# Performance work log

Hardware: AMD Instinct MI355X
Metric: run time of the kernel (lower is better)

Reference implementation:

```python
import jax, jax.numpy as jnp
import numpy as np
import math

NUM_HEADS = 8
SR_RATIO = 2
LN_EPS = 1e-5


def setup_inputs() -> dict:
    key = jax.random.key(0)
    ks = jax.random.split(key, 8)
    B, H, W, C = 2, 64, 64, 512
    N = H * W
    M = (H // SR_RATIO) * (W // SR_RATIO)  # 1024, K/V feature dim after SR reshape
    units = C  # num_heads * head_dim
    s = 0.02
    return {
        "x": jax.random.normal(ks[0], (B, N, C), jnp.float32),
        "Wq": jax.random.normal(ks[1], (C, units), jnp.float32) * s,
        "bq": jnp.zeros((units,), jnp.float32),
        "Wconv": jax.random.normal(ks[2], (C, C, SR_RATIO, SR_RATIO), jnp.float32) * s,  # OIHW
        "bconv": jnp.zeros((C,), jnp.float32),
        "gamma": jnp.ones((M,), jnp.float32),
        "beta": jnp.zeros((M,), jnp.float32),
        "Wkv": jax.random.normal(ks[3], (M, 2 * units), jnp.float32) * s,
        "bkv": jnp.zeros((2 * units,), jnp.float32),
        "Wproj": jax.random.normal(ks[4], (units, C), jnp.float32) * s,
        "bproj": jnp.zeros((C,), jnp.float32),
        "H": H,
        "W": W,
    }


def reference(x, Wq, bq, Wconv, bconv, gamma, beta, Wkv, bkv, Wproj, bproj, H, W):
    B, N, C = x.shape
    nh = NUM_HEADS
    hd = C // nh
    units = nh * hd
    sr = SR_RATIO

    # Q: [B, nh, N, hd]
    q = (x @ Wq + bq).reshape(B, N, nh, hd).transpose(0, 2, 1, 3)

    # Spatial reduction on K/V: x -> [B, C, H, W] -> conv(stride=sr) -> [B, C, H/sr, W/sr]
    xi = x.transpose(0, 2, 1).reshape(B, C, H, W)
    xc = jax.lax.conv_general_dilated(
        xi, Wconv, window_strides=(sr, sr), padding="VALID",
        dimension_numbers=("NCHW", "OIHW", "NCHW"))
    xc = xc + bconv[None, :, None, None]
    x_ = xc.reshape(B, C, -1)  # [B, C, M]; K/V seq len = C, feature dim = M
    mu = jnp.mean(x_, axis=-1, keepdims=True)
    var = jnp.mean(jnp.square(x_ - mu), axis=-1, keepdims=True)
    x_ = (x_ - mu) * jax.lax.rsqrt(var + LN_EPS) * gamma + beta

    # KV: [B, C, 2*units] -> [2, B, nh, C, hd]
    kv = (x_ @ Wkv + bkv).reshape(B, C, 2, nh, hd).transpose(2, 0, 3, 1, 4)
    k, v = kv[0], kv[1]  # each [B, nh, C, hd]

    attn = jnp.einsum("bhnd,bhmd->bhnm", q, k) / jnp.asarray(math.sqrt(hd), x.dtype)
    attn = jax.nn.softmax(attn, axis=-1)  # [B, nh, N, C]

    out = jnp.einsum("bhnm,bhmd->bhnd", attn, v)  # [B, nh, N, hd]
    # Faithful to original: transpose to [B, nh, hd, N] then row-major reshape to [B, N, units]
    out = out.transpose(0, 1, 3, 2).reshape(B, -1, units)
    out = out @ Wproj + bproj  # [B, N, C]
    return out
```

## Files before the change

### kernel.cpp

```cpp
#include <hip/hip_runtime.h>


#define B_    2
#define NTOK  4096
#define C_    512
#define MSP   1024
#define NH    8
#define HD    64

typedef __attribute__((ext_vector_type(8))) short short8;
typedef __attribute__((ext_vector_type(4))) short short4v;
typedef __attribute__((ext_vector_type(4))) float f32x4;

__device__ __forceinline__ unsigned short f2bf(float f) {
    unsigned u = __builtin_bit_cast(unsigned, f);
    u += 0x7FFFu + ((u >> 16) & 1u);
    return (unsigned short)(u >> 16);
}

__global__ __launch_bounds__(256) void convert_bf16(
    const float* __restrict__ in, unsigned short* __restrict__ out, int n8)
{
    int i = blockIdx.x * 256 + threadIdx.x;
    if (i >= n8) return;
    float4 a = ((const float4*)in)[2 * i];
    float4 b = ((const float4*)in)[2 * i + 1];
    short8 o;
    o[0] = (short)f2bf(a.x); o[1] = (short)f2bf(a.y);
    o[2] = (short)f2bf(a.z); o[3] = (short)f2bf(a.w);
    o[4] = (short)f2bf(b.x); o[5] = (short)f2bf(b.y);
    o[6] = (short)f2bf(b.z); o[7] = (short)f2bf(b.w);
    ((short8*)out)[i] = o;
}

__global__ __launch_bounds__(256) void transpose_convert(
    const float* __restrict__ in, unsigned short* __restrict__ out, int R, int C)
{
    __shared__ float T[64][68];
    const int tid = threadIdx.x;
    const int r0 = blockIdx.y * 64, c0 = blockIdx.x * 64;
    const int i = tid >> 2, jp = tid & 3;
    #pragma unroll
    for (int q = 0; q < 4; ++q) {
        float4 v = *(const float4*)(in + (long)(r0 + i) * C + c0 + jp * 16 + q * 4);
        *(float4*)&T[i][jp * 16 + q * 4] = v;
    }
    __syncthreads();
    #pragma unroll
    for (int q = 0; q < 4; ++q) {
        short4v o;
        #pragma unroll
        for (int l = 0; l < 4; ++l)
            o[l] = (short)f2bf(T[jp * 16 + q * 4 + l][i]);
        *(short4v*)(out + (long)(c0 + i) * R + r0 + jp * 16 + q * 4) = o;
    }
}

__global__ __launch_bounds__(256) void gather_kernel(
    const float* __restrict__ x, unsigned short* __restrict__ xg,
    unsigned short* __restrict__ xb)
{
    const int tid = threadIdx.x;
    const int ty = tid >> 4, tx = tid & 15;
    const int m = blockIdx.x * 16 + ty;
    const int b = blockIdx.y;
    const int my = m >> 5, mx = m & 31;
    const float* xb_ = x + (long)b * NTOK * C_;
    unsigned short* op = xg + ((long)b * MSP + m) * 2048;
    unsigned short* xo = xb + (long)b * NTOK * C_;
    const int n00 = (2 * my) * 64 + 2 * mx;
    const int n01 = n00 + 1, n10 = n00 + 64, n11 = n00 + 65;
    const float* p00 = xb_ + (long)n00 * C_;
    const float* p01 = xb_ + (long)n01 * C_;
    const float* p10 = xb_ + (long)n10 * C_;
    const float* p11 = xb_ + (long)n11 * C_;
    for (int c0 = tx * 4; c0 < C_; c0 += 64) {
        float4 v0 = *(const float4*)(p00 + c0);
        float4 v1 = *(const float4*)(p01 + c0);
        float4 v2 = *(const float4*)(p10 + c0);
        float4 v3 = *(const float4*)(p11 + c0);
        short8 o0, o1;
        o0[0] = (short)f2bf(v0.x); o0[1] = (short)f2bf(v1.x);
        o0[2] = (short)f2bf(v2.x); o0[3] = (short)f2bf(v3.x);
        o0[4] = (short)f2bf(v0.y); o0[5] = (short)f2bf(v1.y);
        o0[6] = (short)f2bf(v2.y); o0[7] = (short)f2bf(v3.y);
        o1[0] = (short)f2bf(v0.z); o1[1] = (short)f2bf(v1.z);
        o1[2] = (short)f2bf(v2.z); o1[3] = (short)f2bf(v3.z);
        o1[4] = (short)f2bf(v0.w); o1[5] = (short)f2bf(v1.w);
        o1[6] = (short)f2bf(v2.w); o1[7] = (short)f2bf(v3.w);
        *(short8*)(op + 4 * c0) = o0;
        *(short8*)(op + 4 * c0 + 8) = o1;
        short4v s;
        s[0] = (short)f2bf(v0.x); s[1] = (short)f2bf(v0.y);
        s[2] = (short)f2bf(v0.z); s[3] = (short)f2bf(v0.w);
        *(short4v*)(xo + (long)n00 * C_ + c0) = s;
        s[0] = (short)f2bf(v1.x); s[1] = (short)f2bf(v1.y);
        s[2] = (short)f2bf(v1.z); s[3] = (short)f2bf(v1.w);
        *(short4v*)(xo + (long)n01 * C_ + c0) = s;
        s[0] = (short)f2bf(v2.x); s[1] = (short)f2bf(v2.y);
        s[2] = (short)f2bf(v2.z); s[3] = (short)f2bf(v2.w);
        *(short4v*)(xo + (long)n10 * C_ + c0) = s;
        s[0] = (short)f2bf(v3.x); s[1] = (short)f2bf(v3.y);
        s[2] = (short)f2bf(v3.z); s[3] = (short)f2bf(v3.w);
        *(short4v*)(xo + (long)n11 * C_ + c0) = s;
    }
}

template<int OMODE>
__global__ __launch_bounds__(256) void gemm_bf16(
    const unsigned short* __restrict__ A, const unsigned short* __restrict__ BT,
    const float* __restrict__ bias, void* __restrict__ Cv,
    int M, int N, int Kc, int KS, int lda, int ldb, int ldc,
    long sAb, long sBb, long sCb)
{
    __shared__ unsigned short As[128][72];
    __shared__ unsigned short Bs[128][72];
    const int tid = threadIdx.x;
    const int z = blockIdx.z, b = z / KS, kc = z % KS;
    const int row0 = blockIdx.y * 128, col0 = blockIdx.x * 128;
    const unsigned short* Ap = A + b * sAb + (long)kc * Kc + (long)row0 * lda;
    const unsigned short* Bp = BT + b * sBb + (long)kc * Kc + (long)col0 * ldb;
    const int lane = tid & 63, wave = tid >> 6;
    const int wr = (wave >> 1) * 64, wc = (wave & 1) * 64;
    const int l15 = lane & 15, l4 = lane >> 4;

    f32x4 acc[4][4] = {};
    const int nk = Kc >> 6;
    for (int ks = 0; ks < nk; ++ks) {
        const int k0 = ks << 6;
        short8 ar[4], br[4];
        int rr[4], pp[4];
        #pragma unroll
        for (int i = 0; i < 4; ++i) {
            int chunk = tid + 256 * i;
            rr[i] = chunk >> 3; pp[i] = chunk & 7;
            ar[i] = *(const short8*)(Ap + (long)rr[i] * lda + k0 + pp[i] * 8);
            br[i] = *(const short8*)(Bp + (long)rr[i] * ldb + k0 + pp[i] * 8);
        }
        __syncthreads();
        #pragma unroll
        for (int i = 0; i < 4; ++i) {
            *(short8*)&As[rr[i]][pp[i] * 8] = ar[i];
            *(short8*)&Bs[rr[i]][pp[i] * 8] = br[i];
        }
        __syncthreads();
        #pragma unroll
        for (int kg = 0; kg < 2; ++kg) {
            short8 af[4], bf[4];
            #pragma unroll
            for (int mf = 0; mf < 4; ++mf)
                af[mf] = *(const short8*)&As[wr + mf * 16 + l15][kg * 32 + l4 * 8];
            #pragma unroll
            for (int nf = 0; nf < 4; ++nf)
                bf[nf] = *(const short8*)&Bs[wc + nf * 16 + l15][kg * 32 + l4 * 8];
            #pragma unroll
            for (int mf = 0; mf < 4; ++mf)
                #pragma unroll
                for (int nf = 0; nf < 4; ++nf)
                    acc[mf][nf] = __builtin_amdgcn_mfma_f32_16x16x32_bf16(
                        af[mf], bf[nf], acc[mf][nf], 0, 0, 0);
        }
    }
    const int cb = col0 + wc + l15;
    const int rb = row0 + wr + l4 * 4;
    if (OMODE == 0) {
        float* C = (float*)Cv + (long)z * M * (long)ldc;
        #pragma unroll
        for (int mf = 0; mf < 4; ++mf)
            #pragma unroll
            for (int nf = 0; nf < 4; ++nf)
                #pragma unroll
                for (int i = 0; i < 4; ++i)
                    C[(long)(rb + mf * 16 + i) * ldc + cb + nf * 16] = acc[mf][nf][i];
    } else if (OMODE == 1) {
        unsigned short* C = (unsigned short*)Cv + sCb * b;
        #pragma unroll
        for (int nf = 0; nf < 4; ++nf) {
            float bv = bias[cb + nf * 16];
            #pragma unroll
            for (int mf = 0; mf < 4; ++mf)
                #pragma unroll
                for (int i = 0; i < 4; ++i)
                    C[(long)(rb + mf * 16 + i) * ldc + cb + nf * 16] =
                        f2bf(acc[mf][nf][i] + bv);
        }
    } else {
        float* C = (float*)Cv + sCb * b;
        #pragma unroll
        for (int nf = 0; nf < 4; ++nf) {
            float bv = bias[cb + nf * 16];
            #pragma unroll
            for (int mf = 0; mf < 4; ++mf)
                #pragma unroll
                for (int i = 0; i < 4; ++i)
                    C[(long)(rb + mf * 16 + i) * ldc + cb + nf * 16] =
                        acc[mf][nf][i] + bv;
        }
    }
}

__global__ __launch_bounds__(256) void ln_kernel(
    const float* __restrict__ pconv, unsigned short* __restrict__ xwb,
    const float* __restrict__ gamma, const float* __restrict__ beta)
{
    __shared__ float red[256];
    const int tid = threadIdx.x;
    const int b = blockIdx.x >> 9, c = blockIdx.x & 511;
    const float* base = pconv + ((long)b * 4 * 512 + c) * 1024;
    const int m = tid * 4;
    float4 v = make_float4(0.f, 0.f, 0.f, 0.f);
    #pragma unroll
    for (int kc = 0; kc < 4; ++kc) {
        float4 t = *(const float4*)(base + (long)kc * 512 * 1024 + m);
        v.x += t.x; v.y += t.y; v.z += t.z; v.w += t.w;
    }
    red[tid] = v.x + v.y + v.z + v.w;
    __syncthreads();
    for (int off = 128; off > 0; off >>= 1) {
        if (tid < off) red[tid] += red[tid + off];
        __syncthreads();
    }
    float mu = red[0] * (1.0f / MSP);
    __syncthreads();
    float dx = v.x - mu, dy = v.y - mu, dz = v.z - mu, dw = v.w - mu;
    red[tid] = dx * dx + dy * dy + dz * dz + dw * dw;
    __syncthreads();
    for (int off = 128; off > 0; off >>= 1) {
        if (tid < off) red[tid] += red[tid + off];
        __syncthreads();
    }
    float rs = rsqrtf(red[0] * (1.0f / MSP) + 1e-5f);
    float4 g  = *(const float4*)(gamma + m);
    float4 be = *(const float4*)(beta + m);
    short4v o;
    o[0] = (short)f2bf(dx * rs * g.x + be.x);
    o[1] = (short)f2bf(dy * rs * g.y + be.y);
    o[2] = (short)f2bf(dz * rs * g.z + be.z);
    o[3] = (short)f2bf(dw * rs * g.w + be.w);
    *(short4v*)(xwb + (long)blockIdx.x * MSP + m) = o;
}

__global__ __launch_bounds__(256) void kvpost_kernel(
    const float* __restrict__ pkv, const float* __restrict__ bkv,
    unsigned short* __restrict__ kbuf, unsigned short* __restrict__ vT)
{
    __shared__ float T[64][68];
    const int tid = threadIdx.x;
    const int m0 = blockIdx.x * 64, u0 = blockIdx.y * 64, b = blockIdx.z;
    const float* base = pkv + (long)b * 4 * 512 * 1024;
    const int i = tid >> 2, jp = tid & 3;
    #pragma unroll
    for (int q = 0; q < 4; ++q) {
        int uc = u0 + jp * 16 + q * 4;
        float4 bb = *(const float4*)(bkv + uc);
        float4 v = bb;
        #pragma unroll
        for (int kc = 0; kc < 4; ++kc) {
            float4 t = *(const float4*)(base + (long)kc * 512 * 1024 + (long)(m0 + i) * 1024 + uc);
            v.x += t.x; v.y += t.y; v.z += t.z; v.w += t.w;
        }
        short4v o;
        o[0] = (short)f2bf(v.x); o[1] = (short)f2bf(v.y);
        o[2] = (short)f2bf(v.z); o[3] = (short)f2bf(v.w);
        *(short4v*)(kbuf + ((long)b * 512 + m0 + i) * 512 + uc) = o;
    }
    #pragma unroll
    for (int q = 0; q < 4; ++q) {
        int uc = u0 + jp * 16 + q * 4;
        float4 bb = *(const float4*)(bkv + 512 + uc);
        float4 v = bb;
        #pragma unroll
        for (int kc = 0; kc < 4; ++kc) {
            float4 t = *(const float4*)(base + (long)kc * 512 * 1024 + (long)(m0 + i) * 1024 + 512 + uc);
            v.x += t.x; v.y += t.y; v.z += t.z; v.w += t.w;
        }
        *(float4*)&T[i][jp * 16 + q * 4] = v;
    }
    __syncthreads();
    #pragma unroll
    for (int q = 0; q < 4; ++q) {
        short4v o;
        #pragma unroll
        for (int l = 0; l < 4; ++l)
            o[l] = (short)f2bf(T[jp * 16 + q * 4 + l][i]);
        *(short4v*)(vT + ((long)b * 512 + u0 + i) * 512 + m0 + jp * 16 + q * 4) = o;
    }
}

__global__ __launch_bounds__(256) void attn_kernel(
    const unsigned short* __restrict__ qb, const unsigned short* __restrict__ kbuf,
    const unsigned short* __restrict__ vT, unsigned short* __restrict__ o2)
{
    __shared__ unsigned short Qs[128][72];
    __shared__ unsigned short Ks[64][72];
    __shared__ unsigned short Vs[64][72];
    __shared__ unsigned short Ps[4][32][72];
    const int tid = threadIdx.x;
    const int b = blockIdx.y >> 3, h = blockIdx.y & 7;
    const int n0 = blockIdx.x * 128;
    const int lane = tid & 63, w = tid >> 6;
    const int l15 = lane & 15, l4 = lane >> 4;

    const unsigned short* Qg = qb + ((long)b * NTOK + n0) * 512 + h * 64;
    const unsigned short* Kg = kbuf + (long)b * 512 * 512 + h * 64;
    const unsigned short* Vg = vT + ((long)b * 512 + h * 64) * 512;

    #pragma unroll
    for (int it = 0; it < 4; ++it) {
        int chunk = tid + 256 * it;
        int r = chunk >> 3, p = chunk & 7;
        *(short8*)&Qs[r][p * 8] = *(const short8*)(Qg + (long)r * 512 + p * 8);
    }
    __syncthreads();
    short8 qa[2][2];
    #pragma unroll
    for (int mf = 0; mf < 2; ++mf)
        #pragma unroll
        for (int kg = 0; kg < 2; ++kg)
            qa[mf][kg] = *(const short8*)&Qs[w * 32 + mf * 16 + l15][kg * 32 + l4 * 8];

    f32x4 oacc[2][4] = {};
    float lsum[2][4] = {};

    for (int mt = 0; mt < 8; ++mt) {
        const int m0 = mt * 64;
        __syncthreads();
        #pragma unroll
        for (int it = 0; it < 2; ++it) {
            int chunk = tid + 256 * it;
            int r = chunk >> 3, p = chunk & 7;
            *(short8*)&Ks[r][p * 8] = *(const short8*)(Kg + (long)(m0 + r) * 512 + p * 8);
            *(short8*)&Vs[r][p * 8] = *(const short8*)(Vg + (long)r * 512 + m0 + p * 8);
        }
        __syncthreads();
        f32x4 s[2][4];
        #pragma unroll
        for (int nf = 0; nf < 4; ++nf) {
            short8 kb0 = *(const short8*)&Ks[nf * 16 + l15][l4 * 8];
            short8 kb1 = *(const short8*)&Ks[nf * 16 + l15][32 + l4 * 8];
            #pragma unroll
            for (int mf = 0; mf < 2; ++mf) {
                f32x4 zz = {};
                zz = __builtin_amdgcn_mfma_f32_16x16x32_bf16(qa[mf][0], kb0, zz, 0, 0, 0);
                zz = __builtin_amdgcn_mfma_f32_16x16x32_bf16(qa[mf][1], kb1, zz, 0, 0, 0);
                s[mf][nf] = zz;
            }
        }
        #pragma unroll
        for (int mf = 0; mf < 2; ++mf)
            #pragma unroll
            for (int nf = 0; nf < 4; ++nf)
                #pragma unroll
                for (int i = 0; i < 4; ++i) {
                    float pv = __expf(s[mf][nf][i] * 0.125f);
                    lsum[mf][i] += pv;
                    Ps[w][mf * 16 + l4 * 4 + i][nf * 16 + l15] = f2bf(pv);
                }
        #pragma unroll
        for (int mf = 0; mf < 2; ++mf) {
            short8 pa0 = *(const short8*)&Ps[w][mf * 16 + l15][l4 * 8];
            short8 pa1 = *(const short8*)&Ps[w][mf * 16 + l15][32 + l4 * 8];
            #pragma unroll
            for (int df = 0; df < 4; ++df) {
                short8 vb0 = *(const short8*)&Vs[df * 16 + l15][l4 * 8];
                short8 vb1 = *(const short8*)&Vs[df * 16 + l15][32 + l4 * 8];
                oacc[mf][df] = __builtin_amdgcn_mfma_f32_16x16x32_bf16(pa0, vb0, oacc[mf][df], 0, 0, 0);
                oacc[mf][df] = __builtin_amdgcn_mfma_f32_16x16x32_bf16(pa1, vb1, oacc[mf][df], 0, 0, 0);
            }
        }
    }
    #pragma unroll
    for (int mf = 0; mf < 2; ++mf)
        #pragma unroll
        for (int i = 0; i < 4; ++i) {
            float v = lsum[mf][i];
            v += __shfl_xor(v, 1, 64);
            v += __shfl_xor(v, 2, 64);
            v += __shfl_xor(v, 4, 64);
            v += __shfl_xor(v, 8, 64);
            lsum[mf][i] = 1.0f / v;
        }
    const int nhi = n0 >> 9;
    const int colb = (n0 & 511) + w * 32;
    #pragma unroll
    for (int mf = 0; mf < 2; ++mf)
        #pragma unroll
        for (int df = 0; df < 4; ++df) {
            int d = h * 64 + df * 16 + l15;
            long row = (long)b * NTOK + (long)d * 8 + nhi;
            short4v o;
            o[0] = (short)f2bf(oacc[mf][df][0] * lsum[mf][0]);
            o[1] = (short)f2bf(oacc[mf][df][1] * lsum[mf][1]);
            o[2] = (short)f2bf(oacc[mf][df][2] * lsum[mf][2]);
            o[3] = (short)f2bf(oacc[mf][df][3] * lsum[mf][3]);
            *(short4v*)(o2 + row * 512 + colb + mf * 16 + l4 * 4) = o;
        }
}

extern "C" void kernel_launch(void* const* d_in, const int* in_sizes, int n_in,
                              void* d_out, int out_size, void* d_ws, size_t ws_size,
                              hipStream_t stream)
{
    (void)in_sizes; (void)n_in; (void)out_size; (void)ws_size;
    const float* x     = (const float*)d_in[0];
    const float* Wq    = (const float*)d_in[1];
    const float* bq    = (const float*)d_in[2];
    const float* Wconv = (const float*)d_in[3];
    const float* gamma = (const float*)d_in[5];
    const float* beta  = (const float*)d_in[6];
    const float* Wkv   = (const float*)d_in[7];
    const float* bkv   = (const float*)d_in[8];
    const float* Wproj = (const float*)d_in[9];
    const float* bproj = (const float*)d_in[10];
    float* out = (float*)d_out;
    char* ws = (char*)d_ws;

    unsigned short* xb     = (unsigned short*)(ws);
    unsigned short* qbuf   = (unsigned short*)(ws + (8ul  << 20));
    unsigned short* xg     = (unsigned short*)(ws + (16ul << 20));
    unsigned short* o2     = xg;
    unsigned short* WqT    = (unsigned short*)(ws + (24ul << 20));
    unsigned short* WcB    = (unsigned short*)(ws + (25ul << 20));
    unsigned short* WkvT   = (unsigned short*)(ws + (27ul << 20));
    unsigned short* WprojT = (unsigned short*)(ws + (29ul << 20));
    float*          pconv  = (float*)         (ws + (30ul << 20));
    unsigned short* xwb    = (unsigned short*)(ws + (46ul << 20));
    float*          pkv    = (float*)         (ws + (48ul << 20));
    unsigned short* kbuf   = (unsigned short*)(ws + (64ul << 20));
    unsigned short* vTb    = (unsigned short*)(ws + (65ul << 20));

    convert_bf16<<<dim3(512),  256, 0, stream>>>(Wconv, WcB, 1048576 / 8);
    transpose_convert<<<dim3(8, 8),   256, 0, stream>>>(Wq,    WqT,    512, 512);
    transpose_convert<<<dim3(16, 16), 256, 0, stream>>>(Wkv,   WkvT,   1024, 1024);
    transpose_convert<<<dim3(8, 8),   256, 0, stream>>>(Wproj, WprojT, 512, 512);
    gather_kernel<<<dim3(64, 2), 256, 0, stream>>>(x, xg, xb);

    gemm_bf16<1><<<dim3(4, 64, 1), 256, 0, stream>>>(
        xb, WqT, bq, qbuf, 8192, 512, 512, 1, 512, 512, 512, 0, 0, 0);
    gemm_bf16<0><<<dim3(8, 4, 8), 256, 0, stream>>>(
        WcB, xg, nullptr, pconv, 512, 1024, 512, 4, 2048, 2048, 1024,
        0, 2048l * 1024, 0);
    ln_kernel<<<dim3(1024), 256, 0, stream>>>(pconv, xwb, gamma, beta);
    gemm_bf16<0><<<dim3(8, 4, 8), 256, 0, stream>>>(
        xwb, WkvT, nullptr, pkv, 512, 1024, 256, 4, 1024, 1024, 1024,
        512l * 1024, 0, 0);
    kvpost_kernel<<<dim3(8, 8, 2), 256, 0, stream>>>(pkv, bkv, kbuf, vTb);
    attn_kernel<<<dim3(32, 16), 256, 0, stream>>>(qbuf, kbuf, vTb, o2);
    gemm_bf16<2><<<dim3(4, 64, 1), 256, 0, stream>>>(
        o2, WprojT, bproj, out, 8192, 512, 512, 1, 512, 512, 512, 0, 0, 0);
}
```

Baseline: 192.4 us.

## Fuse prep kernels into one launch and shrink GEMM tiles to 64x64

Merges the four weight conversion/transpose kernels and the gather into a single prep_kernel dispatched by block index, removing four launches. Shrinks the GEMM tile from 128x128 to 64x64 so the Q and projection GEMMs launch 1024 blocks instead of 256, filling more of the CUs. Cuts the split-K factor from 4 to 2 for the conv and KV GEMMs, and updates the LN and kvpost reductions to sum two partials. Smaller tiles lower operand reuse and raise the global and LDS traffic per FLOP.

```diff
diff --git a/kernel.cpp b/kernel.cpp
--- a/kernel.cpp
+++ b/kernel.cpp
@@ -18,27 +18,11 @@
     return (unsigned short)(u >> 16);
 }
 
-__global__ __launch_bounds__(256) void convert_bf16(
-    const float* __restrict__ in, unsigned short* __restrict__ out, int n8)
-{
-    int i = blockIdx.x * 256 + threadIdx.x;
-    if (i >= n8) return;
-    float4 a = ((const float4*)in)[2 * i];
-    float4 b = ((const float4*)in)[2 * i + 1];
-    short8 o;
-    o[0] = (short)f2bf(a.x); o[1] = (short)f2bf(a.y);
-    o[2] = (short)f2bf(a.z); o[3] = (short)f2bf(a.w);
-    o[4] = (short)f2bf(b.x); o[5] = (short)f2bf(b.y);
-    o[6] = (short)f2bf(b.z); o[7] = (short)f2bf(b.w);
-    ((short8*)out)[i] = o;
-}
-
-__global__ __launch_bounds__(256) void transpose_convert(
-    const float* __restrict__ in, unsigned short* __restrict__ out, int R, int C)
-{
-    __shared__ float T[64][68];
-    const int tid = threadIdx.x;
-    const int r0 = blockIdx.y * 64, c0 = blockIdx.x * 64;
+__device__ __forceinline__ void tconv_dev(
+    const float* __restrict__ in, unsigned short* __restrict__ out,
+    int R, int C, int bx, int by, int tid, float (*T)[68])
+{
+    const int r0 = by * 64, c0 = bx * 64;
     const int i = tid >> 2, jp = tid & 3;
     #pragma unroll
     for (int q = 0; q < 4; ++q) {
@@ -56,82 +40,114 @@
     }
 }
 
-__global__ __launch_bounds__(256) void gather_kernel(
+__global__ __launch_bounds__(256) void prep_kernel(
     const float* __restrict__ x, unsigned short* __restrict__ xg,
-    unsigned short* __restrict__ xb)
-{
+    unsigned short* __restrict__ xb,
+    const float* __restrict__ Wq,    unsigned short* __restrict__ WqT,
+    const float* __restrict__ Wkv,   unsigned short* __restrict__ WkvT,
+    const float* __restrict__ Wproj, unsigned short* __restrict__ WprojT,
+    const float* __restrict__ Wconv, unsigned short* __restrict__ WcB)
+{
+    __shared__ float T[64][68];
+    const int bx = blockIdx.x;
     const int tid = threadIdx.x;
-    const int ty = tid >> 4, tx = tid & 15;
-    const int m = blockIdx.x * 16 + ty;
-    const int b = blockIdx.y;
-    const int my = m >> 5, mx = m & 31;
-    const float* xb_ = x + (long)b * NTOK * C_;
-    unsigned short* op = xg + ((long)b * MSP + m) * 2048;
-    unsigned short* xo = xb + (long)b * NTOK * C_;
-    const int n00 = (2 * my) * 64 + 2 * mx;
-    const int n01 = n00 + 1, n10 = n00 + 64, n11 = n00 + 65;
-    const float* p00 = xb_ + (long)n00 * C_;
-    const float* p01 = xb_ + (long)n01 * C_;
-    const float* p10 = xb_ + (long)n10 * C_;
-    const float* p11 = xb_ + (long)n11 * C_;
-    for (int c0 = tx * 4; c0 < C_; c0 += 64) {
-        float4 v0 = *(const float4*)(p00 + c0);
-        float4 v1 = *(const float4*)(p01 + c0);
-        float4 v2 = *(const float4*)(p10 + c0);
-        float4 v3 = *(const float4*)(p11 + c0);
-        short8 o0, o1;
-        o0[0] = (short)f2bf(v0.x); o0[1] = (short)f2bf(v1.x);
-        o0[2] = (short)f2bf(v2.x); o0[3] = (short)f2bf(v3.x);
-        o0[4] = (short)f2bf(v0.y); o0[5] = (short)f2bf(v1.y);
-        o0[6] = (short)f2bf(v2.y); o0[7] = (short)f2bf(v3.y);
-        o1[0] = (short)f2bf(v0.z); o1[1] = (short)f2bf(v1.z);
-        o1[2] = (short)f2bf(v2.z); o1[3] = (short)f2bf(v3.z);
-        o1[4] = (short)f2bf(v0.w); o1[5] = (short)f2bf(v1.w);
-        o1[6] = (short)f2bf(v2.w); o1[7] = (short)f2bf(v3.w);
-        *(short8*)(op + 4 * c0) = o0;
-        *(short8*)(op + 4 * c0 + 8) = o1;
-        short4v s;
-        s[0] = (short)f2bf(v0.x); s[1] = (short)f2bf(v0.y);
-        s[2] = (short)f2bf(v0.z); s[3] = (short)f2bf(v0.w);
-        *(short4v*)(xo + (long)n00 * C_ + c0) = s;
-        s[0] = (short)f2bf(v1.x); s[1] = (short)f2bf(v1.y);
-        s[2] = (short)f2bf(v1.z); s[3] = (short)f2bf(v1.w);
-        *(short4v*)(xo + (long)n01 * C_ + c0) = s;
-        s[0] = (short)f2bf(v2.x); s[1] = (short)f2bf(v2.y);
-        s[2] = (short)f2bf(v2.z); s[3] = (short)f2bf(v2.w);
-        *(short4v*)(xo + (long)n10 * C_ + c0) = s;
-        s[0] = (short)f2bf(v3.x); s[1] = (short)f2bf(v3.y);
-        s[2] = (short)f2bf(v3.z); s[3] = (short)f2bf(v3.w);
-        *(short4v*)(xo + (long)n11 * C_ + c0) = s;
+
+    if (bx < 128) {
+        const int b = bx >> 6;
+        const int ty = tid >> 4, tx = tid & 15;
+        const int m = (bx & 63) * 16 + ty;
+        const int my = m >> 5, mx = m & 31;
+        const float* xsrc = x + (long)b * NTOK * C_;
+        unsigned short* op = xg + ((long)b * MSP + m) * 2048;
+        unsigned short* xo = xb + (long)b * NTOK * C_;
+        const int n00 = (2 * my) * 64 + 2 * mx;
+        const int n01 = n00 + 1, n10 = n00 + 64, n11 = n00 + 65;
+        const float* p00 = xsrc + (long)n00 * C_;
+        const float* p01 = xsrc + (long)n01 * C_;
+        const float* p10 = xsrc + (long)n10 * C_;
+        const float* p11 = xsrc + (long)n11 * C_;
+        for (int c0 = tx * 4; c0 < C_; c0 += 64) {
+            float4 v0 = *(const float4*)(p00 + c0);
+            float4 v1 = *(const float4*)(p01 + c0);
+            float4 v2 = *(const float4*)(p10 + c0);
+            float4 v3 = *(const float4*)(p11 + c0);
+            short8 o0, o1;
+            o0[0] = (short)f2bf(v0.x); o0[1] = (short)f2bf(v1.x);
+            o0[2] = (short)f2bf(v2.x); o0[3] = (short)f2bf(v3.x);
+            o0[4] = (short)f2bf(v0.y); o0[5] = (short)f2bf(v1.y);
+            o0[6] = (short)f2bf(v2.y); o0[7] = (short)f2bf(v3.y);
+            o1[0] = (short)f2bf(v0.z); o1[1] = (short)f2bf(v1.z);
+            o1[2] = (short)f2bf(v2.z); o1[3] = (short)f2bf(v3.z);
+            o1[4] = (short)f2bf(v0.w); o1[5] = (short)f2bf(v1.w);
+            o1[6] = (short)f2bf(v2.w); o1[7] = (short)f2bf(v3.w);
+            *(short8*)(op + 4 * c0) = o0;
+            *(short8*)(op + 4 * c0 + 8) = o1;
+            short4v s;
+            s[0] = (short)f2bf(v0.x); s[1] = (short)f2bf(v0.y);
+            s[2] = (short)f2bf(v0.z); s[3] = (short)f2bf(v0.w);
+            *(short4v*)(xo + (long)n00 * C_ + c0) = s;
+            s[0] = (short)f2bf(v1.x); s[1] = (short)f2bf(v1.y);
+            s[2] = (short)f2bf(v1.z); s[3] = (short)f2bf(v1.w);
+            *(short4v*)(xo + (long)n01 * C_ + c0) = s;
+            s[0] = (short)f2bf(v2.x); s[1] = (short)f2bf(v2.y);
+            s[2] = (short)f2bf(v2.z); s[3] = (short)f2bf(v2.w);
+            *(short4v*)(xo + (long)n10 * C_ + c0) = s;
+            s[0] = (short)f2bf(v3.x); s[1] = (short)f2bf(v3.y);
+            s[2] = (short)f2bf(v3.z); s[3] = (short)f2bf(v3.w);
+            *(short4v*)(xo + (long)n11 * C_ + c0) = s;
+        }
+    } else if (bx < 192) {
+        int sb = bx - 128;
+        tconv_dev(Wq, WqT, 512, 512, sb & 7, sb >> 3, tid, T);
+    } else if (bx < 448) {
+        int sb = bx - 192;
+        tconv_dev(Wkv, WkvT, 1024, 1024, sb & 15, sb >> 4, tid, T);
+    } else if (bx < 512) {
+        int sb = bx - 448;
+        tconv_dev(Wproj, WprojT, 512, 512, sb & 7, sb >> 3, tid, T);
+    } else {
+        int base = (bx - 512) * 256 + tid;
+        #pragma unroll
+        for (int j = 0; j < 4; ++j) {
+            int i = base + j * 32768;
+            float4 a = ((const float4*)Wconv)[2 * i];
+            float4 b = ((const float4*)Wconv)[2 * i + 1];
+            short8 o;
+            o[0] = (short)f2bf(a.x); o[1] = (short)f2bf(a.y);
+            o[2] = (short)f2bf(a.z); o[3] = (short)f2bf(a.w);
+            o[4] = (short)f2bf(b.x); o[5] = (short)f2bf(b.y);
+            o[6] = (short)f2bf(b.z); o[7] = (short)f2bf(b.w);
+            ((short8*)WcB)[i] = o;
+        }
     }
 }
 
 template<int OMODE>
-__global__ __launch_bounds__(256) void gemm_bf16(
+__global__ __launch_bounds__(256) void gemm64(
     const unsigned short* __restrict__ A, const unsigned short* __restrict__ BT,
     const float* __restrict__ bias, void* __restrict__ Cv,
     int M, int N, int Kc, int KS, int lda, int ldb, int ldc,
     long sAb, long sBb, long sCb)
 {
-    __shared__ unsigned short As[128][72];
-    __shared__ unsigned short Bs[128][72];
+    __shared__ unsigned short As[64][72];
+    __shared__ unsigned short Bs[64][72];
     const int tid = threadIdx.x;
     const int z = blockIdx.z, b = z / KS, kc = z % KS;
-    const int row0 = blockIdx.y * 128, col0 = blockIdx.x * 128;
+    const int row0 = blockIdx.y * 64, col0 = blockIdx.x * 64;
     const unsigned short* Ap = A + b * sAb + (long)kc * Kc + (long)row0 * lda;
     const unsigned short* Bp = BT + b * sBb + (long)kc * Kc + (long)col0 * ldb;
     const int lane = tid & 63, wave = tid >> 6;
-    const int wr = (wave >> 1) * 64, wc = (wave & 1) * 64;
+    const int wr = (wave >> 1) * 32, wc = (wave & 1) * 32;
     const int l15 = lane & 15, l4 = lane >> 4;
 
-    f32x4 acc[4][4] = {};
+    f32x4 acc[2][2] = {};
     const int nk = Kc >> 6;
     for (int ks = 0; ks < nk; ++ks) {
         const int k0 = ks << 6;
-        short8 ar[4], br[4];
-        int rr[4], pp[4];
-        #pragma unroll
-        for (int i = 0; i < 4; ++i) {
+        short8 ar[2], br[2];
+        int rr[2], pp[2];
+        #pragma unroll
+        for (int i = 0; i < 2; ++i) {
             int chunk = tid + 256 * i;
             rr[i] = chunk >> 3; pp[i] = chunk & 7;
             ar[i] = *(const short8*)(Ap + (long)rr[i] * lda + k0 + pp[i] * 8);
@@ -139,24 +155,24 @@
         }
         __syncthreads();
         #pragma unroll
-        for (int i = 0; i < 4; ++i) {
+        for (int i = 0; i < 2; ++i) {
             *(short8*)&As[rr[i]][pp[i] * 8] = ar[i];
             *(short8*)&Bs[rr[i]][pp[i] * 8] = br[i];
         }
         __syncthreads();
         #pragma unroll
         for (int kg = 0; kg < 2; ++kg) {
-            short8 af[4], bf[4];
-            #pragma unroll
-            for (int mf = 0; mf < 4; ++mf)
+            short8 af[2], bf[2];
+            #pragma unroll
+            for (int mf = 0; mf < 2; ++mf)
                 af[mf] = *(const short8*)&As[wr + mf * 16 + l15][kg * 32 + l4 * 8];
             #pragma unroll
-            for (int nf = 0; nf < 4; ++nf)
+            for (int nf = 0; nf < 2; ++nf)
                 bf[nf] = *(const short8*)&Bs[wc + nf * 16 + l15][kg * 32 + l4 * 8];
             #pragma unroll
-            for (int mf = 0; mf < 4; ++mf)
+            for (int mf = 0; mf < 2; ++mf)
                 #pragma unroll
-                for (int nf = 0; nf < 4; ++nf)
+                for (int nf = 0; nf < 2; ++nf)
                     acc[mf][nf] = __builtin_amdgcn_mfma_f32_16x16x32_bf16(
                         af[mf], bf[nf], acc[mf][nf], 0, 0, 0);
         }
@@ -166,19 +182,19 @@
     if (OMODE == 0) {
         float* C = (float*)Cv + (long)z * M * (long)ldc;
         #pragma unroll
-        for (int mf = 0; mf < 4; ++mf)
-            #pragma unroll
-            for (int nf = 0; nf < 4; ++nf)
+        for (int mf = 0; mf < 2; ++mf)
+            #pragma unroll
+            for (int nf = 0; nf < 2; ++nf)
                 #pragma unroll
-                for (int i = 0; i < 4; ++i)
+                for (int i = 0; i < 2 * 2; ++i)
                     C[(long)(rb + mf * 16 + i) * ldc + cb + nf * 16] = acc[mf][nf][i];
     } else if (OMODE == 1) {
         unsigned short* C = (unsigned short*)Cv + sCb * b;
         #pragma unroll
-        for (int nf = 0; nf < 4; ++nf) {
+        for (int nf = 0; nf < 2; ++nf) {
             float bv = bias[cb + nf * 16];
             #pragma unroll
-            for (int mf = 0; mf < 4; ++mf)
+            for (int mf = 0; mf < 2; ++mf)
                 #pragma unroll
                 for (int i = 0; i < 4; ++i)
                     C[(long)(rb + mf * 16 + i) * ldc + cb + nf * 16] =
@@ -187,10 +203,10 @@
     } else {
         float* C = (float*)Cv + sCb * b;
         #pragma unroll
-        for (int nf = 0; nf < 4; ++nf) {
+        for (int nf = 0; nf < 2; ++nf) {
             float bv = bias[cb + nf * 16];
             #pragma unroll
-            for (int mf = 0; mf < 4; ++mf)
+            for (int mf = 0; mf < 2; ++mf)
                 #pragma unroll
                 for (int i = 0; i < 4; ++i)
                     C[(long)(rb + mf * 16 + i) * ldc + cb + nf * 16] =
@@ -206,13 +222,14 @@
     __shared__ float red[256];
     const int tid = threadIdx.x;
     const int b = blockIdx.x >> 9, c = blockIdx.x & 511;
-    const float* base = pconv + ((long)b * 4 * 512 + c) * 1024;
+    const float* base = pconv + (long)b * 2 * 512 * 1024 + (long)c * 1024;
     const int m = tid * 4;
-    float4 v = make_float4(0.f, 0.f, 0.f, 0.f);
-    #pragma unroll
-    for (int kc = 0; kc < 4; ++kc) {
-        float4 t = *(const float4*)(base + (long)kc * 512 * 1024 + m);
-        v.x += t.x; v.y += t.y; v.z += t.z; v.w += t.w;
+    float4 v;
+    {
+        float4 t0 = *(const float4*)(base + m);
+        float4 t1 = *(const float4*)(base + 512 * 1024 + m);
+        v.x = t0.x + t1.x; v.y = t0.y + t1.y;
+        v.z = t0.z + t1.z; v.w = t0.w + t1.w;
     }
     red[tid] = v.x + v.y + v.z + v.w;
     __syncthreads();
@@ -247,33 +264,30 @@
     __shared__ float T[64][68];
     const int tid = threadIdx.x;
     const int m0 = blockIdx.x * 64, u0 = blockIdx.y * 64, b = blockIdx.z;
-    const float* base = pkv + (long)b * 4 * 512 * 1024;
+    const float* base = pkv + (long)b * 2 * 512 * 1024;
     const int i = tid >> 2, jp = tid & 3;
     #pragma unroll
     for (int q = 0; q < 4; ++q) {
         int uc = u0 + jp * 16 + q * 4;
         float4 bb = *(const float4*)(bkv + uc);
-        float4 v = bb;
-        #pragma unroll
-        for (int kc = 0; kc < 4; ++kc) {
-            float4 t = *(const float4*)(base + (long)kc * 512 * 1024 + (long)(m0 + i) * 1024 + uc);
-            v.x += t.x; v.y += t.y; v.z += t.z; v.w += t.w;
-        }
+        float4 t0 = *(const float4*)(base + (long)(m0 + i) * 1024 + uc);
+        float4 t1 = *(const float4*)(base + 512 * 1024 + (long)(m0 + i) * 1024 + uc);
         short4v o;
-        o[0] = (short)f2bf(v.x); o[1] = (short)f2bf(v.y);
-        o[2] = (short)f2bf(v.z); o[3] = (short)f2bf(v.w);
+        o[0] = (short)f2bf(t0.x + t1.x + bb.x);
+        o[1] = (short)f2bf(t0.y + t1.y + bb.y);
+        o[2] = (short)f2bf(t0.z + t1.z + bb.z);
+        o[3] = (short)f2bf(t0.w + t1.w + bb.w);
         *(short4v*)(kbuf + ((long)b * 512 + m0 + i) * 512 + uc) = o;
     }
     #pragma unroll
     for (int q = 0; q < 4; ++q) {
         int uc = u0 + jp * 16 + q * 4;
         float4 bb = *(const float4*)(bkv + 512 + uc);
-        float4 v = bb;
-        #pragma unroll
-        for (int kc = 0; kc < 4; ++kc) {
-            float4 t = *(const float4*)(base + (long)kc * 512 * 1024 + (long)(m0 + i) * 1024 + 512 + uc);
-            v.x += t.x; v.y += t.y; v.z += t.z; v.w += t.w;
-        }
+        float4 t0 = *(const float4*)(base + (long)(m0 + i) * 1024 + 512 + uc);
+        float4 t1 = *(const float4*)(base + 512 * 1024 + (long)(m0 + i) * 1024 + 512 + uc);
+        float4 v;
+        v.x = t0.x + t1.x + bb.x; v.y = t0.y + t1.y + bb.y;
+        v.z = t0.z + t1.z + bb.z; v.w = t0.w + t1.w + bb.w;
         *(float4*)&T[i][jp * 16 + q * 4] = v;
     }
     __syncthreads();
@@ -429,23 +443,20 @@
     unsigned short* kbuf   = (unsigned short*)(ws + (64ul << 20));
     unsigned short* vTb    = (unsigned short*)(ws + (65ul << 20));
 
-    convert_bf16<<<dim3(512),  256, 0, stream>>>(Wconv, WcB, 1048576 / 8);
-    transpose_convert<<<dim3(8, 8),   256, 0, stream>>>(Wq,    WqT,    512, 512);
-    transpose_convert<<<dim3(16, 16), 256, 0, stream>>>(Wkv,   WkvT,   1024, 1024);
-    transpose_convert<<<dim3(8, 8),   256, 0, stream>>>(Wproj, WprojT, 512, 512);
-    gather_kernel<<<dim3(64, 2), 256, 0, stream>>>(x, xg, xb);
-
-    gemm_bf16<1><<<dim3(4, 64, 1), 256, 0, stream>>>(
+    prep_kernel<<<dim3(640), 256, 0, stream>>>(
+        x, xg, xb, Wq, WqT, Wkv, WkvT, Wproj, WprojT, Wconv, WcB);
+
+    gemm64<1><<<dim3(8, 128, 1), 256, 0, stream>>>(
         xb, WqT, bq, qbuf, 8192, 512, 512, 1, 512, 512, 512, 0, 0, 0);
-    gemm_bf16<0><<<dim3(8, 4, 8), 256, 0, stream>>>(
-        WcB, xg, nullptr, pconv, 512, 1024, 512, 4, 2048, 2048, 1024,
+    gemm64<0><<<dim3(16, 8, 4), 256, 0, stream>>>(
+        WcB, xg, nullptr, pconv, 512, 1024, 1024, 2, 2048, 2048, 1024,
         0, 2048l * 1024, 0);
     ln_kernel<<<dim3(1024), 256, 0, stream>>>(pconv, xwb, gamma, beta);
-    gemm_bf16<0><<<dim3(8, 4, 8), 256, 0, stream>>>(
-        xwb, WkvT, nullptr, pkv, 512, 1024, 256, 4, 1024, 1024, 1024,
+    gemm64<0><<<dim3(16, 8, 4), 256, 0, stream>>>(
+        xwb, WkvT, nullptr, pkv, 512, 1024, 512, 2, 1024, 1024, 1024,
         512l * 1024, 0, 0);
     kvpost_kernel<<<dim3(8, 8, 2), 256, 0, stream>>>(pkv, bkv, kbuf, vTb);
     attn_kernel<<<dim3(32, 16), 256, 0, stream>>>(qbuf, kbuf, vTb, o2);
-    gemm_bf16<2><<<dim3(4, 64, 1), 256, 0, stream>>>(
+    gemm64<2><<<dim3(8, 128, 1), 256, 0, stream>>>(
         o2, WprojT, bproj, out, 8192, 512, 512, 1, 512, 512, 512, 0, 0, 0);
 }
```

New measurement: 180.2 us. 1.07x faster.
